# Performance work log

Measured on AMD Instinct MI355X. Metric: run time of the kernel, lower is better.

The kernel has to match this reference:

```python
import jax, jax.numpy as jnp
import numpy as np

BS, NUM_R, NUM_P, SL_Q = 32, 10, 36, 20
IMG_FEAT, TOPIC_DIM, LSTM = 2048, 600, 512
CAT = IMG_FEAT + TOPIC_DIM  # 2648


def _w(k, fan_in, shape):
    return jax.random.normal(k, shape, jnp.float32) * (1.0 / np.sqrt(fan_in))


def setup_inputs() -> dict:
    key = jax.random.key(0)
    ks = jax.random.split(key, 12)
    img = jax.random.normal(ks[0], (BS, NUM_P, IMG_FEAT), jnp.float32)
    topic_aggregation = jax.random.normal(ks[1], (BS, NUM_R, SL_Q, TOPIC_DIM), jnp.float32)
    ques_not_pad = jax.random.randint(ks[2], (BS, NUM_R, SL_Q), 0, 2, jnp.int32)
    return {
        "img": img,
        "topic_aggregation": topic_aggregation,
        "ques_not_pad": ques_not_pad,
        # GatedTrans for image: img_feature_size -> lstm_hidden_size
        "Wy_img": _w(ks[3], IMG_FEAT, (IMG_FEAT, LSTM)), "by_img": jnp.zeros((LSTM,), jnp.float32),
        "Wg_img": _w(ks[4], IMG_FEAT, (IMG_FEAT, LSTM)), "bg_img": jnp.zeros((LSTM,), jnp.float32),
        # GatedTrans for topic: 2*word_embedding_size -> lstm_hidden_size
        "Wy_t": _w(ks[5], TOPIC_DIM, (TOPIC_DIM, LSTM)), "by_t": jnp.zeros((LSTM,), jnp.float32),
        "Wg_t": _w(ks[6], TOPIC_DIM, (TOPIC_DIM, LSTM)), "bg_t": jnp.zeros((LSTM,), jnp.float32),
        # MLP: cat -> cat -> img_feat
        "W1": _w(ks[7], CAT, (CAT, CAT)), "b1": jnp.zeros((CAT,), jnp.float32),
        "W2": _w(ks[8], CAT, (CAT, IMG_FEAT)), "b2": jnp.zeros((IMG_FEAT,), jnp.float32),
    }


def _gated(x, Wy, by, Wg, bg):
    # GatedTrans: tanh(Linear) * leaky_relu(Linear); dropout is identity (eval)
    return jnp.tanh(x @ Wy + by) * jax.nn.leaky_relu(x @ Wg + bg, negative_slope=0.01)


def reference(img, topic_aggregation, ques_not_pad,
              Wy_img, by_img, Wg_img, bg_img,
              Wy_t, by_t, Wg_t, bg_t,
              W1, b1, W2, b2):
    bs, num_p, img_feat = img.shape
    _, num_r, sl_q, t_dim = topic_aggregation.shape

    # image GatedTrans is identical across rounds -> compute once, broadcast
    v_feat = _gated(img, Wy_img, by_img, Wg_img, bg_img)            # (bs, num_p, lstm)
    v_feat = jnp.broadcast_to(v_feat[:, None], (bs, num_r, num_p, v_feat.shape[-1]))
    v_feat = v_feat.reshape(bs * num_r, num_p, -1)                  # (B, num_p, lstm)

    topic_feat = _gated(topic_aggregation, Wy_t, by_t, Wg_t, bg_t)
    topic_feat = topic_feat.reshape(bs * num_r, sl_q, -1)           # (B, sl_q, lstm)

    mask = ques_not_pad.reshape(bs * num_r, 1, sl_q).astype(jnp.float32)

    vt_score = jnp.einsum('bpl,bsl->bps', v_feat, topic_feat)       # (B, num_p, sl_q)
    vt_score = vt_score * mask + (mask - 1.0) * 10000.0
    vt_score = jax.nn.softmax(vt_score, axis=-1)

    topic_flat = topic_aggregation.reshape(bs * num_r, sl_q, t_dim)
    # broadcast-multiply+sum in original == bmm over sl_q
    vt_att = jnp.einsum('bps,bst->bpt', vt_score, topic_flat)       # (B, num_p, t_dim)

    img_exp = jnp.broadcast_to(img[:, None], (bs, num_r, num_p, img_feat))
    img_exp = img_exp.reshape(bs * num_r, num_p, img_feat)

    h = jnp.concatenate([img_exp, vt_att], axis=-1)                 # (B, num_p, cat)
    h = jax.nn.relu(h @ W1 + b1)
    h = jax.nn.relu(h @ W2 + b2)
    return h.reshape(bs, num_r, num_p, img_feat)
```

## Files before the change

### kernel.cpp

```cpp
#include <hip/hip_runtime.h>
#include <hip/hip_bf16.h>
#include <cstddef>
#include <cstdint>

#define BS_     32
#define NUM_R_  10
#define NUM_P_  36
#define SL_Q_   20
#define IMG_F_  2048
#define TDIM_   600
#define TDIMP_  640
#define LSTM_   512
#define CAT_    2648
#define CATP_K  2688
#define CATP_R  2688
#define CATP_R8 2816

typedef unsigned short ushort_t;
typedef __attribute__((ext_vector_type(8))) short short8;
typedef __attribute__((ext_vector_type(4))) float f32x4;

__device__ __forceinline__ ushort_t f2bf(float f) {
  union { float f; unsigned int u; } v; v.f = f;
  unsigned int r = v.u + 0x7fff + ((v.u >> 16) & 1);
  return (ushort_t)(r >> 16);
}
__device__ __forceinline__ float bf2f(ushort_t u) {
  union { unsigned int u; float f; } v; v.u = ((unsigned int)u) << 16;
  return v.f;
}

typedef __attribute__((address_space(1))) const unsigned int as1_uint;
typedef __attribute__((address_space(3))) unsigned int as3_uint;
__device__ __forceinline__ void gl_lds16(const ushort_t* g, ushort_t* l) {
  __builtin_amdgcn_global_load_lds((as1_uint*)g, (as3_uint*)l, 16, 0, 0);
}

__device__ __forceinline__ void trans_tile(
    const float* __restrict__ in, ushort_t* __restrict__ out,
    int r0, int R, int C, int Rp, int Cp, int bx, int by)
{
  __shared__ float tile[64][65];
  const int t = threadIdx.x;
  const int lc = t & 63, g = t >> 6;
  const int rbase = by * 64, cbase = bx * 64;
#pragma unroll
  for (int i = 0; i < 16; ++i) {
    int lr = g + 4 * i;
    int rr = rbase + lr, cc = cbase + lc;
    tile[lr][lc] = (rr < R && cc < C) ? in[(size_t)(r0 + rr) * C + cc] : 0.f;
  }
  __syncthreads();
#pragma unroll
  for (int i = 0; i < 16; ++i) {
    int wr2 = g + 4 * i;
    int oc = cbase + wr2, orr = rbase + lc;
    if (oc < Cp && orr < Rp)
      out[(size_t)oc * Rp + orr] = f2bf(tile[lc][wr2]);
  }
}

#define CONV_NB_IMG  2304
#define CONV_NB_TOP  4000
#define CONV_TOTAL   6304
#define TJ1_OFF 0
#define TJ2_OFF 256
#define TJ3_OFF 512
#define TJ4_OFF 592
#define TJ5_OFF 672
#define TJ6_OFF 2016
#define TJ7_OFF 2456
#define TJ_TOTAL 3800
#define PREP_TOTAL (CONV_TOTAL + TJ_TOTAL)

__global__ __launch_bounds__(256) void prep_all_k(
    const float* __restrict__ img, ushort_t* __restrict__ img_bf,
    const float* __restrict__ topic, ushort_t* __restrict__ topic_bf,
    const float* __restrict__ Wy_img, ushort_t* __restrict__ WyT_img,
    const float* __restrict__ Wg_img, ushort_t* __restrict__ WgT_img,
    const float* __restrict__ Wy_t,  ushort_t* __restrict__ WyT_t,
    const float* __restrict__ Wg_t,  ushort_t* __restrict__ WgT_t,
    const float* __restrict__ W1,    ushort_t* __restrict__ W1T_top,
    ushort_t* __restrict__ W1T_bot,
    const float* __restrict__ W2,    ushort_t* __restrict__ W2T)
{
  const int bid0 = blockIdx.x;
  if (bid0 < CONV_NB_IMG) {
    int i = bid0 * 256 + threadIdx.x;
    float4 v = reinterpret_cast<const float4*>(img)[i];
    ushort4 o;
    o.x = f2bf(v.x); o.y = f2bf(v.y); o.z = f2bf(v.z); o.w = f2bf(v.w);
    reinterpret_cast<ushort4*>(img_bf)[i] = o;
    return;
  }
  if (bid0 < CONV_TOTAL) {
    const int npc = TDIMP_ >> 2;
    int i = (bid0 - CONV_NB_IMG) * 256 + threadIdx.x;
    int row = i / npc, c4 = (i - row * npc) << 2;
    ushort4 o = make_ushort4(0, 0, 0, 0);
    if (c4 < TDIM_) {
      float4 v = *reinterpret_cast<const float4*>(&topic[(size_t)row * TDIM_ + c4]);
      o.x = f2bf(v.x); o.y = f2bf(v.y); o.z = f2bf(v.z); o.w = f2bf(v.w);
    }
    *reinterpret_cast<ushort4*>(&topic_bf[(size_t)row * TDIMP_ + c4]) = o;
    return;
  }
  const int bid = bid0 - CONV_TOTAL;
  if (bid < TJ2_OFF) {
    int l = bid - TJ1_OFF;
    trans_tile(Wy_img, WyT_img, 0, 2048, 512, 2048, 512, l % 8, l / 8);
  } else if (bid < TJ3_OFF) {
    int l = bid - TJ2_OFF;
    trans_tile(Wg_img, WgT_img, 0, 2048, 512, 2048, 512, l % 8, l / 8);
  } else if (bid < TJ4_OFF) {
    int l = bid - TJ3_OFF;
    trans_tile(Wy_t, WyT_t, 0, 600, 512, TDIMP_, 512, l % 8, l / 8);
  } else if (bid < TJ5_OFF) {
    int l = bid - TJ4_OFF;
    trans_tile(Wg_t, WgT_t, 0, 600, 512, TDIMP_, 512, l % 8, l / 8);
  } else if (bid < TJ6_OFF) {
    int l = bid - TJ5_OFF;
    trans_tile(W1, W1T_top, 0, 2048, CAT_, 2048, CATP_R, l % 42, l / 42);
  } else if (bid < TJ7_OFF) {
    int l = bid - TJ6_OFF;
    trans_tile(W1, W1T_bot, 2048, 600, CAT_, TDIMP_, CATP_R8, l % 44, l / 44);
  } else {
    int l = bid - TJ7_OFF;
    trans_tile(W2, W2T, 0, CAT_, 2048, CATP_K, 2048, l % 32, l / 32);
  }
}

__device__ __forceinline__ void gated_body(
    ushort_t* __restrict__ smem,
    const ushort_t* __restrict__ A,
    const ushort_t* __restrict__ ByT, const ushort_t* __restrict__ BgT,
    const float* __restrict__ by, const float* __restrict__ bg,
    ushort_t* __restrict__ out, int M, int Kp, int bx, int byi)
{
  ushort_t* Als = smem;
  ushort_t* Bls = smem + 8192;
  const int tid = threadIdx.x;
  const int lane = tid & 63, w = tid >> 6;
  const int wr = w >> 1, wc = w & 1;
  const int m0 = byi * 128, n0 = bx * 64;
  const int N = LSTM_;

  const int srow = lane >> 2;
  const int scol = (lane & 3) * 8;
  const ushort_t* gA0 = A + (size_t)(m0 + w * 32 + srow) * Kp + scol;
  const ushort_t* gA1 = gA0 + (size_t)16 * Kp;
  const ushort_t* gBm = (w >> 1) ? BgT : ByT;
  const ushort_t* gB0 = gBm + (size_t)(n0 + (w & 1) * 32 + srow) * Kp + scol;
  const ushort_t* gB1 = gB0 + (size_t)16 * Kp;
  const int dA0 = (w * 32) * 32, dA1 = (w * 32 + 16) * 32;
  const int dB0 = ((w & 1) * 32) * 32, dB1 = ((w & 1) * 32 + 16) * 32;
  const int bm = w >> 1;

#define STAGE_W(BUF, KOFF) do {                                   \
    gl_lds16(gA0 + (KOFF), Als + (BUF) * 4096 + dA0);             \
    gl_lds16(gA1 + (KOFF), Als + (BUF) * 4096 + dA1);             \
    gl_lds16(gB0 + (KOFF), Bls + (BUF) * 4096 + bm * 2048 + dB0); \
    gl_lds16(gB1 + (KOFF), Bls + (BUF) * 4096 + bm * 2048 + dB1); \
  } while (0)

  f32x4 accy[4][2] = {}, accg[4][2] = {};
  short8 af[4], byf[2], bgf[2];

#define GATED_COMP(BUF) do {                                                  \
    _Pragma("unroll")                                                         \
    for (int i = 0; i < 4; ++i)                                               \
      af[i] = *reinterpret_cast<const short8*>(                               \
          Als + (BUF) * 4096 +                                                \
          (wr * 64 + i * 16 + (lane & 15)) * 32 + (lane >> 4) * 8);           \
    _Pragma("unroll")                                                         \
    for (int j = 0; j < 2; ++j) {                                             \
      int boff = (wc * 32 + j * 16 + (lane & 15)) * 32 + (lane >> 4) * 8;     \
      byf[j] = *reinterpret_cast<const short8*>(Bls + (BUF) * 4096 + boff);   \
      bgf[j] = *reinterpret_cast<const short8*>(Bls + (BUF) * 4096 + 2048 + boff); \
    }                                                                         \
    _Pragma("unroll")                                                         \
    for (int i = 0; i < 4; ++i)                                               \
      _Pragma("unroll")                                                       \
      for (int j = 0; j < 2; ++j) {                                           \
        accy[i][j] = __builtin_amdgcn_mfma_f32_16x16x32_bf16(af[i], byf[j], accy[i][j], 0, 0, 0); \
        accg[i][j] = __builtin_amdgcn_mfma_f32_16x16x32_bf16(af[i], bgf[j], accg[i][j], 0, 0, 0); \
      }                                                                       \
  } while (0)

  STAGE_W(0, 0);
  __syncthreads();
  int kb = 0;
  const int nt2 = Kp >> 6;
  for (int i = 0; i < nt2 - 1; ++i) {
    STAGE_W(1, kb + 32);
    GATED_COMP(0);
    __syncthreads();
    STAGE_W(0, kb + 64);
    GATED_COMP(1);
    __syncthreads();
    kb += 64;
  }
  STAGE_W(1, kb + 32);
  GATED_COMP(0);
  __syncthreads();
  GATED_COMP(1);
#undef STAGE_W
#undef GATED_COMP

  const int crow = (lane >> 4) * 4, ccol = lane & 15;
#pragma unroll
  for (int i = 0; i < 4; ++i)
#pragma unroll
    for (int j = 0; j < 2; ++j)
#pragma unroll
      for (int q = 0; q < 4; ++q) {
        int gm = m0 + wr * 64 + i * 16 + crow + q;
        int gn = n0 + wc * 32 + j * 16 + ccol;
        if (gm >= M || gn >= N) continue;
        float y = tanhf(accy[i][j][q] + by[gn]);
        float g = accg[i][j][q] + bg[gn];
        g = (g > 0.f) ? g : 0.01f * g;
        out[(size_t)gm * N + gn] = f2bf(y * g);
      }
}

__device__ __forceinline__ void gemm128_body(
    ushort_t* __restrict__ smem,
    const ushort_t* __restrict__ A, const ushort_t* __restrict__ BT,
    float* __restrict__ outf, int M, int Kp, int N, int bx, int by)
{
  ushort_t* Als = smem;
  ushort_t* Bls = smem + 8192;
  const int tid = threadIdx.x;
  const int lane = tid & 63, w = tid >> 6;
  const int wr = w >> 1, wc = w & 1;
  const int m0 = by * 128, n0 = bx * 128;

  const int srow = lane >> 2;
  const int scol = (lane & 3) * 8;
  const ushort_t* gA0 = A + (size_t)(m0 + w * 32 + srow) * Kp + scol;
  const ushort_t* gA1 = gA0 + (size_t)16 * Kp;
  const ushort_t* gB0 = BT + (size_t)(n0 + w * 32 + srow) * Kp + scol;
  const ushort_t* gB1 = gB0 + (size_t)16 * Kp;
  const int d0 = (w * 32) * 32, d1 = (w * 32 + 16) * 32;

#define STAGE_G(BUF, KOFF) do {                           \
    gl_lds16(gA0 + (KOFF), Als + (BUF) * 4096 + d0);      \
    gl_lds16(gA1 + (KOFF), Als + (BUF) * 4096 + d1);      \
    gl_lds16(gB0 + (KOFF), Bls + (BUF) * 4096 + d0);      \
    gl_lds16(gB1 + (KOFF), Bls + (BUF) * 4096 + d1);      \
  } while (0)

  f32x4 acc[4][4] = {};
  short8 af[4], bfv[4];

#define GEMM_COMP(BUF) do {                                                   \
    _Pragma("unroll")                                                         \
    for (int i = 0; i < 4; ++i)                                               \
      af[i] = *reinterpret_cast<const short8*>(                               \
          Als + (BUF) * 4096 +                                                \
          (wr * 64 + i * 16 + (lane & 15)) * 32 + (lane >> 4) * 8);           \
    _Pragma("unroll")                                                         \
    for (int j = 0; j < 4; ++j)                                               \
      bfv[j] = *reinterpret_cast<const short8*>(                              \
          Bls + (BUF) * 4096 +                                                \
          (wc * 64 + j * 16 + (lane & 15)) * 32 + (lane >> 4) * 8);           \
    _Pragma("unroll")                                                         \
    for (int i = 0; i < 4; ++i)                                               \
      _Pragma("unroll")                                                       \
      for (int j = 0; j < 4; ++j)                                             \
        acc[i][j] = __builtin_amdgcn_mfma_f32_16x16x32_bf16(af[i], bfv[j], acc[i][j], 0, 0, 0); \
  } while (0)

  STAGE_G(0, 0);
  __syncthreads();
  int kb = 0;
  const int nt2 = Kp >> 6;
  for (int i = 0; i < nt2 - 1; ++i) {
    STAGE_G(1, kb + 32);
    GEMM_COMP(0);
    __syncthreads();
    STAGE_G(0, kb + 64);
    GEMM_COMP(1);
    __syncthreads();
    kb += 64;
  }
  STAGE_G(1, kb + 32);
  GEMM_COMP(0);
  __syncthreads();
  GEMM_COMP(1);
#undef STAGE_G
#undef GEMM_COMP

  const int crow = (lane >> 4) * 4, ccol = lane & 15;
#pragma unroll
  for (int i = 0; i < 4; ++i)
#pragma unroll
    for (int j = 0; j < 4; ++j)
#pragma unroll
      for (int q = 0; q < 4; ++q) {
        int gm = m0 + wr * 64 + i * 16 + crow + q;
        int gn = n0 + wc * 64 + j * 16 + ccol;
        if (gm < M && gn < N) outf[(size_t)gm * N + gn] = acc[i][j][q];
      }
}

#define GB_IMG 72
#define GB_TOP 400
#define HB_NB  189
#define MID_TOTAL (GB_IMG + GB_TOP + HB_NB)

__global__ __launch_bounds__(256) void mid_all_k(
    const ushort_t* __restrict__ img_bf,
    const ushort_t* __restrict__ WyT_img, const ushort_t* __restrict__ WgT_img,
    const float* __restrict__ by_img, const float* __restrict__ bg_img,
    ushort_t* __restrict__ v_feat,
    const ushort_t* __restrict__ topic_bf,
    const ushort_t* __restrict__ WyT_t, const ushort_t* __restrict__ WgT_t,
    const float* __restrict__ by_t, const float* __restrict__ bg_t,
    ushort_t* __restrict__ topic_ft,
    const ushort_t* __restrict__ W1T_top, float* __restrict__ himg)
{
  __shared__ ushort_t smem[16384];
  const int bid = blockIdx.x;
  if (bid < GB_IMG) {
    gated_body(smem, img_bf, WyT_img, WgT_img, by_img, bg_img, v_feat,
               1152, 2048, bid & 7, bid >> 3);
  } else if (bid < GB_IMG + GB_TOP) {
    const int l = bid - GB_IMG;
    gated_body(smem, topic_bf, WyT_t, WgT_t, by_t, bg_t, topic_ft,
               6400, TDIMP_, l & 7, l >> 3);
  } else {
    const int l = bid - GB_IMG - GB_TOP;
    gemm128_body(smem, img_bf, W1T_top, himg, 1152, 2048, CAT_,
                 l % 21, l / 21);
  }
}

__global__ __launch_bounds__(512, 2) void mfma_gemm8_k(
    const ushort_t* __restrict__ A, const ushort_t* __restrict__ BT,
    const float* __restrict__ bias, const float* __restrict__ D,
    float* __restrict__ outf, ushort_t* __restrict__ outb,
    int M, int Kp, int N, int ldOutb, int mode, int base)
{
  extern __shared__ ushort_t lds8[];
  const int tid = threadIdx.x;
  const int lane = tid & 63, w = tid >> 6;
  const int wr = w >> 2, wc = w & 3;
  const int m0 = blockIdx.y * 256, n0 = blockIdx.x * 256;
  const int r15 = lane & 15, lg = lane >> 4;

  const int pr = lane >> 3, hh = lane & 7;
  const int cc = hh ^ pr;
  const int srow_l = (pr << 1) | (cc >> 2);
  const int scol_l = (cc & 3) << 3;

#define STAGE8(b_, s_, kt_) do {                                             \
    const ushort_t* src_ = ((s_) & 1) ? BT : A;                              \
    const int rowb_ = ((s_) & 1) ? n0 : m0;                                  \
    const int kcol_ = (kt_) * 64 + ((s_) >> 1) * 32 + scol_l;                \
    ushort_t* dst_ = &lds8[(b_) * 32768 + (s_) * 8192];                      \
    _Pragma("unroll")                                                        \
    for (int i_ = 0; i_ < 2; ++i_) {                                         \
      int grow_ = rowb_ + w * 32 + i_ * 16 + srow_l;                         \
      gl_lds16(src_ + (size_t)grow_ * Kp + kcol_,                            \
               &dst_[(w * 32 + i_ * 16) * 32]);                              \
    }                                                                        \
  } while (0)

#define LDS_RD(b_, s_, row_) (*reinterpret_cast<const short8*>(              \
    &lds8[(b_) * 32768 + (s_) * 8192 + ((row_) >> 1) * 64 +                  \
          (((((row_) & 1) << 2) | lg) ^ (((row_) >> 1) & 7)) * 8]))

  f32x4 acc[8][4] = {};
  short8 aR0[8], aR1[8];
  short8 bR0[2], bR1[2];
  const int NT = Kp >> 6;

#define PHASE_WAIT() do {                                   \
    asm volatile("s_waitcnt vmcnt(4)" ::: "memory");        \
    __builtin_amdgcn_s_barrier();                           \
    __builtin_amdgcn_sched_barrier(0);                      \
  } while (0)

#define PRELOAD_A(ar_, b_, ks_) do {                                        \
    _Pragma("unroll")                                                       \
    for (int mf_ = 0; mf_ < 8; ++mf_)                                       \
      ar_[mf_] = LDS_RD(b_, (ks_) * 2, wr * 128 + mf_ * 16 + r15);          \
  } while (0)

#define PRELOAD_B(br_, b_, ks_, nfb_) do {                                  \
    br_[0] = LDS_RD(b_, (ks_) * 2 + 1, wc * 64 + (nfb_) * 16 + r15);        \
    br_[1] = LDS_RD(b_, (ks_) * 2 + 1, wc * 64 + ((nfb_) + 1) * 16 + r15);  \
  } while (0)

#define MFMA_G(ar_, br_, nfb_) do {                                         \
    __builtin_amdgcn_sched_barrier(0);                                      \
    __builtin_amdgcn_s_setprio(1);                                          \
    _Pragma("unroll")                                                       \
    for (int mf_ = 0; mf_ < 8; ++mf_) {                                     \
      acc[mf_][(nfb_)] = __builtin_amdgcn_mfma_f32_16x16x32_bf16(           \
          ar_[mf_], br_[0], acc[mf_][(nfb_)], 0, 0, 0);                     \
      acc[mf_][(nfb_) + 1] = __builtin_amdgcn_mfma_f32_16x16x32_bf16(       \
          ar_[mf_], br_[1], acc[mf_][(nfb_) + 1], 0, 0, 0);                 \
    }                                                                       \
    __builtin_amdgcn_s_setprio(0);                                          \
    __builtin_amdgcn_sched_barrier(0);                                      \
  } while (0)

  STAGE8(0, 0, 0); STAGE8(0, 1, 0); STAGE8(0, 2, 0); STAGE8(0, 3, 0);
  asm volatile("s_waitcnt vmcnt(0)" ::: "memory");
  __builtin_amdgcn_s_barrier();
  __builtin_amdgcn_sched_barrier(0);
  PRELOAD_A(aR0, 0, 0);
  PRELOAD_B(bR0, 0, 0, 0);

  for (int T = 0; T < NT - 1; ++T) {
    const int b = T & 1, nb = b ^ 1;
    STAGE8(nb, 0, T + 1);
    PHASE_WAIT();
    PRELOAD_B(bR1, b, 0, 2);
    MFMA_G(aR0, bR0, 0);
    STAGE8(nb, 1, T + 1);
    PHASE_WAIT();
    PRELOAD_A(aR1, b, 1);
    PRELOAD_B(bR0, b, 1, 0);
    MFMA_G(aR0, bR1, 2);
    STAGE8(nb, 2, T + 1);
    PHASE_WAIT();
    PRELOAD_B(bR1, b, 1, 2);
    MFMA_G(aR1, bR0, 0);
    STAGE8(nb, 3, T + 1);
    PHASE_WAIT();
    PRELOAD_A(aR0, nb, 0);
    PRELOAD_B(bR0, nb, 0, 0);
    MFMA_G(aR1, bR1, 2);
  }
  {
    asm volatile("s_waitcnt vmcnt(0)" ::: "memory");
    __builtin_amdgcn_s_barrier();
    __builtin_amdgcn_sched_barrier(0);
    const int b = (NT - 1) & 1;
    PRELOAD_B(bR1, b, 0, 2);
    MFMA_G(aR0, bR0, 0);
    PRELOAD_A(aR1, b, 1);
    PRELOAD_B(bR0, b, 1, 0);
    MFMA_G(aR0, bR1, 2);
    PRELOAD_B(bR1, b, 1, 2);
    MFMA_G(aR1, bR0, 0);
    MFMA_G(aR1, bR1, 2);
  }
#undef STAGE8
#undef PHASE_WAIT
#undef PRELOAD_A
#undef PRELOAD_B
#undef MFMA_G
#undef LDS_RD

  const int crow = lg * 4;
#pragma unroll
  for (int mf = 0; mf < 8; ++mf) {
#pragma unroll
    for (int nf = 0; nf < 4; ++nf) {
#pragma unroll
      for (int q = 0; q < 4; ++q) {
        int gm = m0 + wr * 128 + mf * 16 + crow + q;
        int gn = n0 + wc * 64 + nf * 16 + r15;
        if (gm >= M) continue;
        float v = acc[mf][nf][q];
        if (mode == 1) {
          if (gn < ldOutb) {
            float vv = 0.f;
            if (gn < N) {
              int g = base + gm;
              int drow = (g / 360) * 36 + (g % 36);
              vv = v + D[(size_t)drow * CAT_ + gn] + bias[gn];
              vv = vv > 0.f ? vv : 0.f;
            }
            outb[(size_t)gm * ldOutb + gn] = f2bf(vv);
          }
        } else {
          if (gn < N) {
            float vv = v + bias[gn];
            outf[(size_t)gm * N + gn] = vv > 0.f ? vv : 0.f;
          }
        }
      }
    }
  }
}

__global__ __launch_bounds__(256) void attn_fuse_k(
    const ushort_t* __restrict__ v_feat,
    const ushort_t* __restrict__ topic_feat,
    const float* __restrict__ topic_raw,
    const int*   __restrict__ qnp,
    ushort_t* __restrict__ vt_att)
{
  const int b  = blockIdx.x;
  const int ib = b / NUM_R_;
  __shared__ float tr[SL_Q_][TDIM_];
  __shared__ float msk[SL_Q_];

  const int tid = threadIdx.x;
  {
    const float4* g = reinterpret_cast<const float4*>(topic_raw + (size_t)b * SL_Q_ * TDIM_);
    float4* s = reinterpret_cast<float4*>(&tr[0][0]);
    for (int i = tid; i < SL_Q_ * TDIM_ / 4; i += 256) s[i] = g[i];
  }
  if (tid < SL_Q_) msk[tid] = (float)qnp[b * SL_Q_ + tid];
  __syncthreads();

  const int wave = tid >> 6, lane = tid & 63;
  const ushort_t* tf_b = topic_feat + (size_t)b * SL_Q_ * LSTM_;

  for (int p = wave; p < NUM_P_; p += 4) {
    const ushort_t* v = v_feat + ((size_t)ib * NUM_P_ + p) * LSTM_;
    float vr[8];
    {
      short8 vv = *reinterpret_cast<const short8*>(&v[lane * 8]);
#pragma unroll
      for (int k = 0; k < 8; ++k) vr[k] = bf2f((ushort_t)vv[k]);
    }

    float sc[SL_Q_];
#pragma unroll
    for (int s = 0; s < SL_Q_; ++s) {
      short8 tv = *reinterpret_cast<const short8*>(&tf_b[(size_t)s * LSTM_ + lane * 8]);
      float acc = 0.f;
#pragma unroll
      for (int k = 0; k < 8; ++k) acc += vr[k] * bf2f((ushort_t)tv[k]);
#pragma unroll
      for (int off = 32; off > 0; off >>= 1) acc += __shfl_xor(acc, off, 64);
      sc[s] = acc;
    }
    float mx = -1e30f;
#pragma unroll
    for (int s = 0; s < SL_Q_; ++s) {
      float m = msk[s];
      sc[s] = sc[s] * m + (m - 1.f) * 10000.f;
      mx = fmaxf(mx, sc[s]);
    }
    float sum = 0.f;
#pragma unroll
    for (int s = 0; s < SL_Q_; ++s) { sc[s] = expf(sc[s] - mx); sum += sc[s]; }
    const float inv = 1.f / sum;

    ushort_t* outp = vt_att + ((size_t)b * NUM_P_ + p) * TDIMP_;
    for (int t = lane; t < TDIMP_; t += 64) {
      float acc = 0.f;
      if (t < TDIM_) {
#pragma unroll
        for (int s = 0; s < SL_Q_; ++s) acc += sc[s] * tr[s][t];
        acc *= inv;
      }
      outp[t] = f2bf(t < TDIM_ ? acc : 0.f);
    }
  }
}

extern "C" void kernel_launch(void* const* d_in, const int* in_sizes, int n_in,
                              void* d_out, int out_size, void* d_ws, size_t ws_size,
                              hipStream_t stream) {
  const float* img    = (const float*)d_in[0];
  const float* topic  = (const float*)d_in[1];
  const int*   qnp    = (const int*)d_in[2];
  const float* Wy_img = (const float*)d_in[3];
  const float* by_img = (const float*)d_in[4];
  const float* Wg_img = (const float*)d_in[5];
  const float* bg_img = (const float*)d_in[6];
  const float* Wy_t   = (const float*)d_in[7];
  const float* by_t   = (const float*)d_in[8];
  const float* Wg_t   = (const float*)d_in[9];
  const float* bg_t   = (const float*)d_in[10];
  const float* W1     = (const float*)d_in[11];
  const float* b1     = (const float*)d_in[12];
  const float* W2     = (const float*)d_in[13];
  const float* b2     = (const float*)d_in[14];
  float* out = (float*)d_out;

  char* base = (char*)d_ws;
  size_t off = 0;
  auto alloc = [&](size_t bytes) {
    void* p = base + off;
    off += (bytes + 255) & ~(size_t)255;
    return p;
  };
  ushort_t* img_bf    = (ushort_t*)alloc((size_t)1152 * 2048 * 2);
  ushort_t* topic_bf  = (ushort_t*)alloc((size_t)6400 * TDIMP_ * 2);
  ushort_t* WyT_img   = (ushort_t*)alloc((size_t)512 * 2048 * 2);
  ushort_t* WgT_img   = (ushort_t*)alloc((size_t)512 * 2048 * 2);
  ushort_t* WyT_t     = (ushort_t*)alloc((size_t)512 * TDIMP_ * 2);
  ushort_t* WgT_t     = (ushort_t*)alloc((size_t)512 * TDIMP_ * 2);
  ushort_t* W1T_top   = (ushort_t*)alloc((size_t)CATP_R * 2048 * 2);
  ushort_t* v_feat    = (ushort_t*)alloc((size_t)1152 * 512 * 2);
  ushort_t* topic_ft  = (ushort_t*)alloc((size_t)6400 * 512 * 2);
  ushort_t* W1T_bot   = (ushort_t*)alloc((size_t)CATP_R8 * TDIMP_ * 2);
  ushort_t* W2T       = (ushort_t*)alloc((size_t)2048 * CATP_K * 2);
  ushort_t* vt_att    = (ushort_t*)alloc((size_t)(11520 + 128) * TDIMP_ * 2);
  float*    himg      = (float*)alloc((size_t)1152 * CAT_ * 4);
  ushort_t* h1c       = (ushort_t*)base;
  (void)ws_size;

  const dim3 blk(256);

  prep_all_k<<<dim3(PREP_TOTAL), blk, 0, stream>>>(
      img, img_bf, topic, topic_bf,
      Wy_img, WyT_img, Wg_img, WgT_img, Wy_t, WyT_t, Wg_t, WgT_t,
      W1, W1T_top, W1T_bot, W2, W2T);

  mid_all_k<<<dim3(MID_TOTAL), blk, 0, stream>>>(
      img_bf, WyT_img, WgT_img, by_img, bg_img, v_feat,
      topic_bf, WyT_t, WgT_t, by_t, bg_t, topic_ft,
      W1T_top, himg);

  attn_fuse_k<<<dim3(BS_ * NUM_R_), blk, 0, stream>>>(v_feat, topic_ft, topic, qnp, vt_att);

  for (int c = 0; c < 2; ++c) {
    const int mbase = c * 5760;
    mfma_gemm8_k<<<dim3(11, 23), dim3(512), 131072, stream>>>(
        vt_att + (size_t)mbase * TDIMP_, W1T_bot, b1, himg, nullptr, h1c,
        5760, TDIMP_, CAT_, CATP_K, 1, mbase);
    mfma_gemm8_k<<<dim3(8, 23), dim3(512), 131072, stream>>>(
        h1c, W2T, b2, nullptr, out + (size_t)mbase * IMG_F_, nullptr,
        5760, CATP_K, 2048, 0, 2, 0);
  }
}
```

Measured before the change: 446.4 us.

## Overlap second-chunk layer-1 GEMM with first-chunk layer-2 GEMM in one launch

The GEMM body becomes a device function so that one launch can run both the layer-2 GEMM of the first row chunk and the layer-1 GEMM of the second chunk. Their block ranges are split by block index. This fills the GPU with more concurrent blocks than either under-sized GEMM grid does alone, and it removes one serial launch boundary. It needs a second intermediate buffer in the workspace and falls back to the old serial loop when the workspace is too small.

```diff
diff --git a/kernel.cpp b/kernel.cpp
--- a/kernel.cpp
+++ b/kernel.cpp
@@ -337,17 +337,17 @@
   }
 }
 
-__global__ __launch_bounds__(512, 2) void mfma_gemm8_k(
+__device__ __forceinline__ void gemm8_body(
+    ushort_t* __restrict__ lds8, int bx, int by,
     const ushort_t* __restrict__ A, const ushort_t* __restrict__ BT,
     const float* __restrict__ bias, const float* __restrict__ D,
     float* __restrict__ outf, ushort_t* __restrict__ outb,
     int M, int Kp, int N, int ldOutb, int mode, int base)
 {
-  extern __shared__ ushort_t lds8[];
   const int tid = threadIdx.x;
   const int lane = tid & 63, w = tid >> 6;
   const int wr = w >> 2, wc = w & 3;
-  const int m0 = blockIdx.y * 256, n0 = blockIdx.x * 256;
+  const int m0 = by * 256, n0 = bx * 256;
   const int r15 = lane & 15, lg = lane >> 4;
 
   const int pr = lane >> 3, hh = lane & 7;
@@ -490,6 +490,38 @@
   }
 }
 
+__global__ __launch_bounds__(512, 2) void mfma_gemm8_k(
+    const ushort_t* __restrict__ A, const ushort_t* __restrict__ BT,
+    const float* __restrict__ bias, const float* __restrict__ D,
+    float* __restrict__ outf, ushort_t* __restrict__ outb,
+    int M, int Kp, int N, int ldOutb, int mode, int base)
+{
+  extern __shared__ ushort_t lds8[];
+  gemm8_body(lds8, blockIdx.x, blockIdx.y, A, BT, bias, D, outf, outb,
+             M, Kp, N, ldOutb, mode, base);
+}
+
+#define EF_F_NB 184
+#define EF_E_NB 253
+__global__ __launch_bounds__(512, 2) void ef_fused_k(
+    const ushort_t* __restrict__ h1c0, const ushort_t* __restrict__ W2T,
+    const float* __restrict__ b2, float* __restrict__ outF,
+    const ushort_t* __restrict__ vtE, const ushort_t* __restrict__ W1T_bot,
+    const float* __restrict__ b1, const float* __restrict__ himg,
+    ushort_t* __restrict__ h1c1, int baseE)
+{
+  extern __shared__ ushort_t lds8[];
+  const int bid = blockIdx.x;
+  if (bid < EF_F_NB) {
+    gemm8_body(lds8, bid & 7, bid >> 3, h1c0, W2T, b2, nullptr,
+               outF, nullptr, 5760, CATP_K, 2048, 0, 2, 0);
+  } else {
+    const int l = bid - EF_F_NB;
+    gemm8_body(lds8, l % 11, l / 11, vtE, W1T_bot, b1, himg,
+               nullptr, h1c1, 5760, TDIMP_, CAT_, CATP_K, 1, baseE);
+  }
+}
+
 __global__ __launch_bounds__(256) void attn_fuse_k(
     const ushort_t* __restrict__ v_feat,
     const ushort_t* __restrict__ topic_feat,
@@ -590,8 +622,8 @@
   ushort_t* topic_bf  = (ushort_t*)alloc((size_t)6400 * TDIMP_ * 2);
   ushort_t* WyT_img   = (ushort_t*)alloc((size_t)512 * 2048 * 2);
   ushort_t* WgT_img   = (ushort_t*)alloc((size_t)512 * 2048 * 2);
-  ushort_t* WyT_t     = (ushort_t*)alloc((size_t)512 * TDIMP_ * 2);
-  ushort_t* WgT_t     = (ushort_t*)alloc((size_t)512 * TDIMP_ * 2);
+  ushort_t* WyT_t    = (ushort_t*)alloc((size_t)512 * TDIMP_ * 2);
+  ushort_t* WgT_t    = (ushort_t*)alloc((size_t)512 * TDIMP_ * 2);
   ushort_t* W1T_top   = (ushort_t*)alloc((size_t)CATP_R * 2048 * 2);
   ushort_t* v_feat    = (ushort_t*)alloc((size_t)1152 * 512 * 2);
   ushort_t* topic_ft  = (ushort_t*)alloc((size_t)6400 * 512 * 2);
@@ -599,8 +631,11 @@
   ushort_t* W2T       = (ushort_t*)alloc((size_t)2048 * CATP_K * 2);
   ushort_t* vt_att    = (ushort_t*)alloc((size_t)(11520 + 128) * TDIMP_ * 2);
   float*    himg      = (float*)alloc((size_t)1152 * CAT_ * 4);
-  ushort_t* h1c       = (ushort_t*)base;
-  (void)ws_size;
+  size_t off_base = off;
+  ushort_t* h1c1      = (ushort_t*)alloc((size_t)5888 * CATP_K * 2);
+  const bool overlap = (ws_size >= off);
+  (void)off_base;
+  ushort_t* h1c0      = (ushort_t*)base;
 
   const dim3 blk(256);
 
@@ -616,13 +651,25 @@
 
   attn_fuse_k<<<dim3(BS_ * NUM_R_), blk, 0, stream>>>(v_feat, topic_ft, topic, qnp, vt_att);
 
-  for (int c = 0; c < 2; ++c) {
-    const int mbase = c * 5760;
+  if (overlap) {
     mfma_gemm8_k<<<dim3(11, 23), dim3(512), 131072, stream>>>(
-        vt_att + (size_t)mbase * TDIMP_, W1T_bot, b1, himg, nullptr, h1c,
-        5760, TDIMP_, CAT_, CATP_K, 1, mbase);
+        vt_att, W1T_bot, b1, himg, nullptr, h1c0,
+        5760, TDIMP_, CAT_, CATP_K, 1, 0);
+    ef_fused_k<<<dim3(EF_F_NB + EF_E_NB), dim3(512), 131072, stream>>>(
+        h1c0, W2T, b2, out,
+        vt_att + (size_t)5760 * TDIMP_, W1T_bot, b1, himg, h1c1, 5760);
     mfma_gemm8_k<<<dim3(8, 23), dim3(512), 131072, stream>>>(
-        h1c, W2T, b2, nullptr, out + (size_t)mbase * IMG_F_, nullptr,
+        h1c1, W2T, b2, nullptr, out + (size_t)5760 * IMG_F_, nullptr,
         5760, CATP_K, 2048, 0, 2, 0);
-  }
-}
+  } else {
+    for (int c = 0; c < 2; ++c) {
+      const int mbase = c * 5760;
+      mfma_gemm8_k<<<dim3(11, 23), dim3(512), 131072, stream>>>(
+          vt_att + (size_t)mbase * TDIMP_, W1T_bot, b1, himg, nullptr, h1c0,
+          5760, TDIMP_, CAT_, CATP_K, 1, mbase);
+      mfma_gemm8_k<<<dim3(8, 23), dim3(512), 131072, stream>>>(
+          h1c0, W2T, b2, nullptr, out + (size_t)mbase * IMG_F_, nullptr,
+          5760, CATP_K, 2048, 0, 2, 0);
+    }
+  }
+}
```

Result: slower. 472.8 us (+5.9%).
